# Kernel tuning notes

Hardware: AMD Instinct MI355X
Metric: run time of the kernel (lower is better)

## Reference

```python
import jax, jax.numpy as jnp
import numpy as np

B, N, M = 8, 4096, 4096


def setup_inputs() -> dict:
    key = jax.random.key(0)
    k1, k2 = jax.random.split(key)
    tar = jax.random.normal(k1, (B, N, 3), dtype=jnp.float32)
    src = jax.random.normal(k2, (B, M, 3), dtype=jnp.float32)
    return {"tar": tar, "src": src}


def reference(tar, src):
    # diff: [b, n, m, 3]; dist: [b, n, m] Euclidean norm
    diff = tar[:, :, None, :] - src[:, None, :, :]
    dist = jnp.sqrt(jnp.sum(diff * diff, axis=-1))
    # complete: for each target point, min over source points, mean over n -> [b]
    complete = jnp.mean(jnp.min(dist, axis=2), axis=1)
    # accuracy: for each source point, min over target points, mean over m -> [b]
    accuracy = jnp.mean(jnp.min(dist, axis=1), axis=1)
    # reduction='mean' over batch axis
    complete = jnp.mean(complete, axis=-1)
    accuracy = jnp.mean(accuracy, axis=-1)
    chamfer = 0.5 * (complete + accuracy)
    return (accuracy, complete, chamfer)
```

## Files before the change

kernel.cpp:

```cpp
#include <hip/hip_runtime.h>
#include <math.h>

#define B_ 8


template <int QPT, int CHUNK>
__global__ __launch_bounds__(256) void minsq_kernel(
    const float* __restrict__ tar, const float* __restrict__ src,
    float* __restrict__ ws, int N, int M)
{
    const int z   = blockIdx.z;
    const int dir = (z >= B_) ? 1 : 0;
    const int b   = dir ? (z - B_) : z;
    const float* __restrict__ qry = dir ? src : tar;
    const float* __restrict__ pts = dir ? tar : src;
    const int K = dir ? M : N;
    const int L = dir ? N : M;

    const int base = blockIdx.y * CHUNK;
    if (base >= L) return;
    const int cnt = min(CHUNK, L - base);

    const size_t slabStride = (size_t)B_ * (N + M);
    float* __restrict__ out = ws + (size_t)blockIdx.y * slabStride
                                 + (dir ? (size_t)B_ * N : (size_t)0)
                                 + (size_t)b * K;

    __shared__ float4 sp[CHUNK];
    const float* __restrict__ psrc = pts + ((size_t)b * L + base) * 3;
    const int t = threadIdx.x;
    for (int i = t; i < cnt; i += 256) {
        float px = psrc[3 * i + 0];
        float py = psrc[3 * i + 1];
        float pz = psrc[3 * i + 2];
        sp[i] = make_float4(px, py, pz, fmaf(px, px, fmaf(py, py, pz * pz)));
    }
    __syncthreads();

    const int qbase = blockIdx.x * (256 * QPT);
    float qx2[QPT], qy2[QPT], qz2[QPT], qw[QPT], mn[QPT];
#pragma unroll
    for (int k = 0; k < QPT; ++k) {
        int qi = qbase + k * 256 + t;
        if (qi < K) {
            const float* qp = qry + ((size_t)b * K + qi) * 3;
            float x = qp[0], y = qp[1], zc = qp[2];
            qx2[k] = -2.f * x; qy2[k] = -2.f * y; qz2[k] = -2.f * zc;
            qw[k] = fmaf(x, x, fmaf(y, y, zc * zc));
        } else {
            qx2[k] = 0.f; qy2[k] = 0.f; qz2[k] = 0.f; qw[k] = 0.f;
        }
        mn[k] = 3.4e38f;
    }

    if (cnt == CHUNK) {
#pragma unroll 4
        for (int j = 0; j < CHUNK; j += 2) {
            float4 p0 = sp[j];
            float4 p1 = sp[j + 1];
#pragma unroll
            for (int k = 0; k < QPT; ++k) {
                float d0 = fmaf(qx2[k], p0.x,
                           fmaf(qy2[k], p0.y,
                           fmaf(qz2[k], p0.z, p0.w)));
                float d1 = fmaf(qx2[k], p1.x,
                           fmaf(qy2[k], p1.y,
                           fmaf(qz2[k], p1.z, p1.w)));
                mn[k] = fminf(mn[k], fminf(d0, d1));
            }
        }
    } else {
        int j = 0;
        for (; j + 1 < cnt; j += 2) {
            float4 p0 = sp[j];
            float4 p1 = sp[j + 1];
#pragma unroll
            for (int k = 0; k < QPT; ++k) {
                float d0 = fmaf(qx2[k], p0.x,
                           fmaf(qy2[k], p0.y,
                           fmaf(qz2[k], p0.z, p0.w)));
                float d1 = fmaf(qx2[k], p1.x,
                           fmaf(qy2[k], p1.y,
                           fmaf(qz2[k], p1.z, p1.w)));
                mn[k] = fminf(mn[k], fminf(d0, d1));
            }
        }
        if (j < cnt) {
            float4 p0 = sp[j];
#pragma unroll
            for (int k = 0; k < QPT; ++k) {
                float d0 = fmaf(qx2[k], p0.x,
                           fmaf(qy2[k], p0.y,
                           fmaf(qz2[k], p0.z, p0.w)));
                mn[k] = fminf(mn[k], d0);
            }
        }
    }

#pragma unroll
    for (int k = 0; k < QPT; ++k) {
        int qi = qbase + k * 256 + t;
        if (qi < K) {
            out[qi] = fmaxf(mn[k] + qw[k], 0.f);
        }
    }
}

template <int CHUNK>
__global__ __launch_bounds__(256) void reduce_kernel(
    const float* __restrict__ ws, float* __restrict__ outp, int N, int M)
{
    const int nt = B_ * N;
    const int ns = B_ * M;
    const size_t slabStride = (size_t)B_ * (N + M);
    const int nslab0 = (M + CHUNK - 1) / CHUNK;
    const int nslab1 = (N + CHUNK - 1) / CHUNK;

    const int gid = blockIdx.x * 256 + threadIdx.x;
    const int stride = gridDim.x * 256;

    float s_t = 0.f, s_s = 0.f;
    for (int i = gid; i < nt; i += stride) {
        float m = ws[i];
        for (int s = 1; s < nslab0; ++s) m = fminf(m, ws[s * slabStride + i]);
        s_t += sqrtf(m);
    }
    for (int i = gid; i < ns; i += stride) {
        const size_t off = (size_t)nt + i;
        float m = ws[off];
        for (int s = 1; s < nslab1; ++s) m = fminf(m, ws[s * slabStride + off]);
        s_s += sqrtf(m);
    }

#pragma unroll
    for (int off = 32; off > 0; off >>= 1) {
        s_t += __shfl_down(s_t, off);
        s_s += __shfl_down(s_s, off);
    }
    __shared__ float rt[4], rs[4];
    const int wid = threadIdx.x >> 6, lid = threadIdx.x & 63;
    if (lid == 0) { rt[wid] = s_t; rs[wid] = s_s; }
    __syncthreads();
    if (threadIdx.x == 0) {
        float ct = (rt[0] + rt[1] + rt[2] + rt[3]) / (float)nt;
        float ac = (rs[0] + rs[1] + rs[2] + rs[3]) / (float)ns;
        atomicAdd(&outp[0], ac);
        atomicAdd(&outp[1], ct);
        atomicAdd(&outp[2], 0.5f * (ac + ct));
    }
}

extern "C" void kernel_launch(void* const* d_in, const int* in_sizes, int n_in,
                              void* d_out, int out_size, void* d_ws, size_t ws_size,
                              hipStream_t stream) {
    const float* tar = (const float*)d_in[0];
    const float* src = (const float*)d_in[1];
    const int N = in_sizes[0] / (B_ * 3);
    const int M = in_sizes[1] / (B_ * 3);
    float* ws = (float*)d_ws;
    float* outp = (float*)d_out;

    hipMemsetAsync(outp, 0, (size_t)out_size * sizeof(float), stream);

    constexpr int QPT = 4, CHUNK = 512;
    const int KL = (N > M) ? N : M;
    const int gx = (KL + 256 * QPT - 1) / (256 * QPT);
    const int gy = (KL + CHUNK - 1) / CHUNK;
    dim3 grid(gx, gy, 2 * B_);
    minsq_kernel<QPT, CHUNK><<<grid, dim3(256), 0, stream>>>(tar, src, ws, N, M);

    reduce_kernel<CHUNK><<<dim3(128), dim3(256), 0, stream>>>(ws, outp, N, M);
}
```

Before: 91.35 us.

## Prepack points as float4 and merge chunk minima with atomicMin

Adds a pack kernel that converts points to float4 with a precomputed squared norm, and moves the output zeroing into that kernel. The min-distance kernel now merges partial minima with an unsigned atomicMin on float bits into a single array instead of writing per-chunk slabs. This cuts workspace traffic, lets the reduce kernel read a single value per point, and removes the memset launch. QPT and CHUNK also change (8/128), which alters the grid shape and register pressure. In exchange it adds a kernel launch and atomic contention on the merged array.

```diff
diff --git a/kernel.cpp b/kernel.cpp
--- a/kernel.cpp
+++ b/kernel.cpp
@@ -2,39 +2,52 @@
 #include <math.h>
 
 #define B_ 8
+#define BIGF 3.4e38f
 
+
+__global__ __launch_bounds__(256) void pack_kernel(
+    const float* __restrict__ tar, const float* __restrict__ src,
+    float4* __restrict__ packT, float4* __restrict__ packS,
+    unsigned int* __restrict__ minarr, float* __restrict__ outp,
+    int N, int M)
+{
+    const int i = blockIdx.x * 256 + threadIdx.x;
+    const int nT = B_ * N, nS = B_ * M;
+    if (i < nT) {
+        float x = tar[3 * i], y = tar[3 * i + 1], z = tar[3 * i + 2];
+        packT[i] = make_float4(x, y, z, fmaf(x, x, fmaf(y, y, z * z)));
+    } else if (i < nT + nS) {
+        int j = i - nT;
+        float x = src[3 * j], y = src[3 * j + 1], z = src[3 * j + 2];
+        packS[j] = make_float4(x, y, z, fmaf(x, x, fmaf(y, y, z * z)));
+    }
+    if (i < nT + nS) minarr[i] = 0x7F800000u;
+    if (i < 3) outp[i] = 0.f;
+}
 
 template <int QPT, int CHUNK>
 __global__ __launch_bounds__(256) void minsq_kernel(
-    const float* __restrict__ tar, const float* __restrict__ src,
-    float* __restrict__ ws, int N, int M)
+    const float4* __restrict__ packT, const float4* __restrict__ packS,
+    unsigned int* __restrict__ minarr, int N, int M)
 {
     const int z   = blockIdx.z;
     const int dir = (z >= B_) ? 1 : 0;
     const int b   = dir ? (z - B_) : z;
-    const float* __restrict__ qry = dir ? src : tar;
-    const float* __restrict__ pts = dir ? tar : src;
+    const float4* __restrict__ qry = dir ? packS : packT;
+    const float4* __restrict__ pts = dir ? packT : packS;
     const int K = dir ? M : N;
     const int L = dir ? N : M;
+    unsigned int* __restrict__ out =
+        minarr + (dir ? (size_t)B_ * N : (size_t)0) + (size_t)b * K;
 
     const int base = blockIdx.y * CHUNK;
     if (base >= L) return;
     const int cnt = min(CHUNK, L - base);
 
-    const size_t slabStride = (size_t)B_ * (N + M);
-    float* __restrict__ out = ws + (size_t)blockIdx.y * slabStride
-                                 + (dir ? (size_t)B_ * N : (size_t)0)
-                                 + (size_t)b * K;
-
     __shared__ float4 sp[CHUNK];
-    const float* __restrict__ psrc = pts + ((size_t)b * L + base) * 3;
+    const float4* __restrict__ psrc = pts + (size_t)b * L + base;
     const int t = threadIdx.x;
-    for (int i = t; i < cnt; i += 256) {
-        float px = psrc[3 * i + 0];
-        float py = psrc[3 * i + 1];
-        float pz = psrc[3 * i + 2];
-        sp[i] = make_float4(px, py, pz, fmaf(px, px, fmaf(py, py, pz * pz)));
-    }
+    for (int i = t; i < cnt; i += 256) sp[i] = psrc[i];
     __syncthreads();
 
     const int qbase = blockIdx.x * (256 * QPT);
@@ -43,14 +56,13 @@
     for (int k = 0; k < QPT; ++k) {
         int qi = qbase + k * 256 + t;
         if (qi < K) {
-            const float* qp = qry + ((size_t)b * K + qi) * 3;
-            float x = qp[0], y = qp[1], zc = qp[2];
-            qx2[k] = -2.f * x; qy2[k] = -2.f * y; qz2[k] = -2.f * zc;
-            qw[k] = fmaf(x, x, fmaf(y, y, zc * zc));
+            float4 q = qry[(size_t)b * K + qi];
+            qx2[k] = -2.f * q.x; qy2[k] = -2.f * q.y; qz2[k] = -2.f * q.z;
+            qw[k] = q.w;
         } else {
             qx2[k] = 0.f; qy2[k] = 0.f; qz2[k] = 0.f; qw[k] = 0.f;
         }
-        mn[k] = 3.4e38f;
+        mn[k] = BIGF;
     }
 
     if (cnt == CHUNK) {
@@ -60,11 +72,9 @@
             float4 p1 = sp[j + 1];
 #pragma unroll
             for (int k = 0; k < QPT; ++k) {
-                float d0 = fmaf(qx2[k], p0.x,
-                           fmaf(qy2[k], p0.y,
+                float d0 = fmaf(qx2[k], p0.x, fmaf(qy2[k], p0.y,
                            fmaf(qz2[k], p0.z, p0.w)));
-                float d1 = fmaf(qx2[k], p1.x,
-                           fmaf(qy2[k], p1.y,
+                float d1 = fmaf(qx2[k], p1.x, fmaf(qy2[k], p1.y,
                            fmaf(qz2[k], p1.z, p1.w)));
                 mn[k] = fminf(mn[k], fminf(d0, d1));
             }
@@ -76,11 +86,9 @@
             float4 p1 = sp[j + 1];
 #pragma unroll
             for (int k = 0; k < QPT; ++k) {
-                float d0 = fmaf(qx2[k], p0.x,
-                           fmaf(qy2[k], p0.y,
+                float d0 = fmaf(qx2[k], p0.x, fmaf(qy2[k], p0.y,
                            fmaf(qz2[k], p0.z, p0.w)));
-                float d1 = fmaf(qx2[k], p1.x,
-                           fmaf(qy2[k], p1.y,
+                float d1 = fmaf(qx2[k], p1.x, fmaf(qy2[k], p1.y,
                            fmaf(qz2[k], p1.z, p1.w)));
                 mn[k] = fminf(mn[k], fminf(d0, d1));
             }
@@ -89,8 +97,7 @@
             float4 p0 = sp[j];
 #pragma unroll
             for (int k = 0; k < QPT; ++k) {
-                float d0 = fmaf(qx2[k], p0.x,
-                           fmaf(qy2[k], p0.y,
+                float d0 = fmaf(qx2[k], p0.x, fmaf(qy2[k], p0.y,
                            fmaf(qz2[k], p0.z, p0.w)));
                 mn[k] = fminf(mn[k], d0);
             }
@@ -101,37 +108,24 @@
     for (int k = 0; k < QPT; ++k) {
         int qi = qbase + k * 256 + t;
         if (qi < K) {
-            out[qi] = fmaxf(mn[k] + qw[k], 0.f);
+            float d2 = fmaxf(mn[k] + qw[k], 0.f);
+            atomicMin(&out[qi], __float_as_uint(d2));
         }
     }
 }
 
-template <int CHUNK>
 __global__ __launch_bounds__(256) void reduce_kernel(
-    const float* __restrict__ ws, float* __restrict__ outp, int N, int M)
+    const unsigned int* __restrict__ minarr, float* __restrict__ outp,
+    int N, int M)
 {
-    const int nt = B_ * N;
-    const int ns = B_ * M;
-    const size_t slabStride = (size_t)B_ * (N + M);
-    const int nslab0 = (M + CHUNK - 1) / CHUNK;
-    const int nslab1 = (N + CHUNK - 1) / CHUNK;
-
+    const int nt = B_ * N, ns = B_ * M;
     const int gid = blockIdx.x * 256 + threadIdx.x;
     const int stride = gridDim.x * 256;
-
     float s_t = 0.f, s_s = 0.f;
-    for (int i = gid; i < nt; i += stride) {
-        float m = ws[i];
-        for (int s = 1; s < nslab0; ++s) m = fminf(m, ws[s * slabStride + i]);
-        s_t += sqrtf(m);
-    }
-    for (int i = gid; i < ns; i += stride) {
-        const size_t off = (size_t)nt + i;
-        float m = ws[off];
-        for (int s = 1; s < nslab1; ++s) m = fminf(m, ws[s * slabStride + off]);
-        s_s += sqrtf(m);
-    }
-
+    for (int i = gid; i < nt; i += stride)
+        s_t += sqrtf(__uint_as_float(minarr[i]));
+    for (int i = gid; i < ns; i += stride)
+        s_s += sqrtf(__uint_as_float(minarr[nt + i]));
 #pragma unroll
     for (int off = 32; off > 0; off >>= 1) {
         s_t += __shfl_down(s_t, off);
@@ -157,17 +151,22 @@
     const float* src = (const float*)d_in[1];
     const int N = in_sizes[0] / (B_ * 3);
     const int M = in_sizes[1] / (B_ * 3);
-    float* ws = (float*)d_ws;
+
+    float4* packT = (float4*)d_ws;
+    float4* packS = packT + (size_t)B_ * N;
+    unsigned int* minarr = (unsigned int*)(packS + (size_t)B_ * M);
     float* outp = (float*)d_out;
 
-    hipMemsetAsync(outp, 0, (size_t)out_size * sizeof(float), stream);
+    pack_kernel<<<dim3((B_ * (N + M) + 255) / 256), dim3(256), 0, stream>>>(
+        tar, src, packT, packS, minarr, outp, N, M);
 
-    constexpr int QPT = 4, CHUNK = 512;
+    constexpr int QPT = 8, CHUNK = 128;
     const int KL = (N > M) ? N : M;
     const int gx = (KL + 256 * QPT - 1) / (256 * QPT);
     const int gy = (KL + CHUNK - 1) / CHUNK;
     dim3 grid(gx, gy, 2 * B_);
-    minsq_kernel<QPT, CHUNK><<<grid, dim3(256), 0, stream>>>(tar, src, ws, N, M);
+    minsq_kernel<QPT, CHUNK><<<grid, dim3(256), 0, stream>>>(
+        packT, packS, minarr, N, M);
 
-    reduce_kernel<CHUNK><<<dim3(128), dim3(256), 0, stream>>>(ws, outp, N, M);
+    reduce_kernel<<<dim3(32), dim3(256), 0, stream>>>(minarr, outp, N, M);
 }
```

Measured after the change: 84.09 us (median of 3 runs). 8.0% less time.
